# Performance work log

Measured on AMD Instinct MI355X. Metric: run time of the kernel, lower is better.

Reference implementation:

```python
import jax, jax.numpy as jnp
import numpy as np

B, S, E = 2, 2048, 2048
H, KV, D = 16, 4, 128


def setup_inputs() -> dict:
    key = jax.random.key(0)
    k0, k1, k2, k3, k4 = jax.random.split(key, 5)
    s = 0.02  # init scale for weights
    return {
        "x": jax.random.normal(k0, (B, S, E), jnp.float32),
        "wq": jax.random.normal(k1, (E, H * D), jnp.float32) * s,
        "wk": jax.random.normal(k2, (E, KV * D), jnp.float32) * s,
        "wv": jax.random.normal(k3, (E, KV * D), jnp.float32) * s,
        "wo": jax.random.normal(k4, (H * D, E), jnp.float32) * s,
    }


def _rope_tables(seq_len, head_dim, dtype):
    inv_freq = 1.0 / (10000.0 ** (jnp.arange(0, head_dim, 2, dtype=jnp.float32) / head_dim))
    t = jnp.arange(seq_len, dtype=jnp.float32)
    freqs = jnp.outer(t, inv_freq)  # [S, D/2]
    emb = jnp.concatenate([freqs, freqs], axis=-1)  # [S, D]
    cos = jnp.cos(emb).astype(dtype)[None, None]  # [1,1,S,D]
    sin = jnp.sin(emb).astype(dtype)[None, None]
    return cos, sin


def _rotate_half(x):
    x1, x2 = jnp.split(x, 2, axis=-1)
    return jnp.concatenate([-x2, x1], axis=-1)


def reference(x, wq, wk, wv, wo):
    b, s, _ = x.shape
    # projections -> [B, heads, S, D]
    q = (x @ wq).reshape(b, s, H, D).transpose(0, 2, 1, 3)
    k = (x @ wk).reshape(b, s, KV, D).transpose(0, 2, 1, 3)
    v = (x @ wv).reshape(b, s, KV, D).transpose(0, 2, 1, 3)
    # inline RoPE (rotate-half convention), applied to q and k
    cos, sin = _rope_tables(s, D, q.dtype)
    q = q * cos + _rotate_half(q) * sin
    k = k * cos + _rotate_half(k) * sin
    # GQA: duplicate K/V heads (repeat_interleave along head dim)
    rep = H // KV
    k = jnp.repeat(k, rep, axis=1)
    v = jnp.repeat(v, rep, axis=1)
    scale = 1.0 / np.sqrt(D)
    scores = jnp.einsum('bhqd,bhkd->bhqk', q, k) * scale  # [B,H,S,S]
    attn = jax.nn.softmax(scores.astype(jnp.float32), axis=-1).astype(q.dtype)
    out = jnp.einsum('bhqk,bhkd->bhqd', attn, v)  # [B,H,S,D]
    out = out.transpose(0, 2, 1, 3).reshape(b, s, H * D)
    return out @ wo
```

## Files before the change

kernel.cpp:

```cpp
#include <hip/hip_runtime.h>
#include <hip/hip_bf16.h>

typedef __attribute__((ext_vector_type(8))) short s16x8;
typedef __attribute__((ext_vector_type(4))) float f32x4;

__device__ inline float bf2f(unsigned short u) {
  union { unsigned int i; float f; } v; v.i = ((unsigned int)u) << 16; return v.f;
}
__device__ inline unsigned short f2bf(float f) {
  union { float f; unsigned int i; } v; v.f = f;
  unsigned int r = (v.i + 0x7FFFu + ((v.i >> 16) & 1u)) >> 16;
  return (unsigned short)r;
}
__device__ inline void gl_lds16(const void* g, void* l) {
  __builtin_amdgcn_global_load_lds(
      (const __attribute__((address_space(1))) unsigned int*)g,
      (__attribute__((address_space(3))) unsigned int*)l, 16, 0, 0);
}

__global__ __launch_bounds__(256) void cast_to_bf16(const float* __restrict__ s,
                                                    unsigned short* __restrict__ d, int n4) {
  int i = blockIdx.x * 256 + threadIdx.x;
  if (i >= n4) return;
  float4 v = ((const float4*)s)[i];
  ushort4 o;
  o.x = f2bf(v.x); o.y = f2bf(v.y); o.z = f2bf(v.z); o.w = f2bf(v.w);
  ((ushort4*)d)[i] = o;
}

__global__ __launch_bounds__(256) void transpose_cast(const float* __restrict__ src,
                                                      unsigned short* __restrict__ dst,
                                                      int K, int N) {
  __shared__ float tile[32][33];
  int n0 = blockIdx.x * 32, k0 = blockIdx.y * 32;
  int tx = threadIdx.x & 31, ty = threadIdx.x >> 5;
#pragma unroll
  for (int i = 0; i < 4; ++i) {
    int k = ty + i * 8;
    tile[k][tx] = src[(size_t)(k0 + k) * N + n0 + tx];
  }
  __syncthreads();
#pragma unroll
  for (int i = 0; i < 4; ++i) {
    int n = ty + i * 8;
    dst[(size_t)(n0 + n) * K + k0 + tx] = f2bf(tile[tx][n]);
  }
}

__global__ __launch_bounds__(256) void rope_tables(float* __restrict__ ct, float* __restrict__ st) {
  int idx = blockIdx.x * 256 + threadIdx.x;
  int s = idx >> 6, i = idx & 63;
  float inv = powf(10000.0f, -(float)(2 * i) * (1.0f / 128.0f));
  float ang = (float)s * inv;
  ct[idx] = cosf(ang);
  st[idx] = sinf(ang);
}

__global__ __launch_bounds__(256) void rope_apply(unsigned short* __restrict__ qkv,
                                                  const float* __restrict__ ct,
                                                  const float* __restrict__ st) {
  int row = blockIdx.x;
  int pos = row & 2047;
  unsigned short* base = qkv + (size_t)row * 3072;
  for (int it = threadIdx.x; it < 1280; it += 256) {
    int head = it >> 6, dh = it & 63;
    int col = head < 16 ? head * 128 : 2048 + (head - 16) * 128;
    float a = bf2f(base[col + dh]);
    float b = bf2f(base[col + dh + 64]);
    float c = ct[pos * 64 + dh], sn = st[pos * 64 + dh];
    base[col + dh] = f2bf(a * c - b * sn);
    base[col + dh + 64] = f2bf(b * c + a * sn);
  }
}

__global__ __launch_bounds__(256) void vtrans(const unsigned short* __restrict__ qkv,
                                              unsigned short* __restrict__ vt) {
  __shared__ unsigned short tile[32][33];
  int tx = threadIdx.x & 31, ty = threadIdx.x >> 5;
  int s0 = blockIdx.x * 32;
  int d0 = blockIdx.y * 32;
  int bz = blockIdx.z;
  const unsigned short* src = qkv + (size_t)((bz >> 2) * 2048) * 3072 + 2560 + (bz & 3) * 128;
#pragma unroll
  for (int i = 0; i < 4; ++i)
    tile[ty + i * 8][tx] = src[(size_t)(s0 + ty + i * 8) * 3072 + d0 + tx];
  __syncthreads();
  unsigned short* dst = vt + (size_t)bz * 128 * 2048;
#pragma unroll
  for (int i = 0; i < 4; ++i)
    dst[(size_t)(d0 + ty + i * 8) * 2048 + s0 + tx] = tile[tx][ty + i * 8];
}

template <int BF16OUT>
__global__ __launch_bounds__(512, 2) void gemm256(const unsigned short* __restrict__ A,
                                                  const unsigned short* __restrict__ BT,
                                                  void* __restrict__ Cv,
                                                  int M, int N, int K) {
  __shared__ __align__(16) unsigned short Lds[2][4][256 * 32];
  const int t = threadIdx.x, lane = t & 63;
  const int wid = t >> 6, m16 = lane & 15, l4 = lane >> 4;
  const int wm = wid >> 2, wn = wid & 3;
  const int swA = (l4 ^ ((m16 >> 1) & 3)) * 16;

  int gx = gridDim.x, nwg = gx * gridDim.y;
  int wg = blockIdx.y * gx + blockIdx.x;
  if ((nwg & 7) == 0) { int q = nwg >> 3; wg = (wg & 7) * q + (wg >> 3); }
  const int rowBase = (wg / gx) * 256, colBase = (wg % gx) * 256;

  const int r0 = t >> 2, c80 = (t & 3) ^ ((r0 >> 1) & 3);
  const int g1 = 512 + t, r1 = g1 >> 2, c81 = (g1 & 3) ^ ((r1 >> 1) & 3);
  const char* pA0 = (const char*)(A + (size_t)(rowBase + r0) * K + c80 * 8);
  const char* pA1 = (const char*)(A + (size_t)(rowBase + r1) * K + c81 * 8);
  const char* pB0 = (const char*)(BT + (size_t)(colBase + r0) * K + c80 * 8);
  const char* pB1 = (const char*)(BT + (size_t)(colBase + r1) * K + c81 * 8);

  f32x4 acc[8][4];
#pragma unroll
  for (int fr = 0; fr < 8; ++fr)
#pragma unroll
    for (int fn = 0; fn < 4; ++fn) {
      f32x4 z = {0.f, 0.f, 0.f, 0.f};
      acc[fr][fn] = z;
    }
  s16x8 bf[4];

#define STG(mat, kc, kt, buf)                                             \
  {                                                                       \
    size_t ko = (size_t)((kt) * 64 + (kc) * 32) * 2;                      \
    char* pl = (char*)&Lds[buf][(mat) * 2 + (kc)][0];                     \
    gl_lds16(((mat) ? pB0 : pA0) + ko, pl + t * 16);                      \
    gl_lds16(((mat) ? pB1 : pA1) + ko, pl + 8192 + t * 16);               \
  }

#define GATE()                                         \
  asm volatile("s_waitcnt vmcnt(8)" ::: "memory");     \
  __builtin_amdgcn_s_barrier();                        \
  __builtin_amdgcn_sched_barrier(0);

#define CMP(cur, kc, frh)                                                          \
  {                                                                                \
    const char* Ap = (const char*)&Lds[cur][kc][0];                                \
    s16x8 af[4];                                                                   \
    _Pragma("unroll") for (int i = 0; i < 4; ++i)                                  \
        af[i] = *(const s16x8*)(Ap + (wm * 128 + ((frh) * 4 + i) * 16 + m16) * 64 + swA); \
    if ((frh) == 0) {                                                              \
      const char* Bp = (const char*)&Lds[cur][2 + (kc)][0];                        \
      _Pragma("unroll") for (int n = 0; n < 4; ++n)                                \
          bf[n] = *(const s16x8*)(Bp + (wn * 64 + n * 16 + m16) * 64 + swA);       \
    }                                                                              \
    __builtin_amdgcn_s_setprio(1);                                                 \
    _Pragma("unroll") for (int i = 0; i < 4; ++i)                                  \
        _Pragma("unroll") for (int n = 0; n < 4; ++n)                              \
            acc[(frh) * 4 + i][n] = __builtin_amdgcn_mfma_f32_16x16x32_bf16(       \
                af[i], bf[n], acc[(frh) * 4 + i][n], 0, 0, 0);                     \
    __builtin_amdgcn_s_setprio(0);                                                 \
  }

  const int NT = K >> 6;
  STG(0, 0, 0, 0); STG(1, 0, 0, 0);
  STG(0, 1, 0, 0); STG(1, 1, 0, 0);
  STG(0, 0, 1, 1); STG(1, 0, 1, 1);

  for (int kt = 0; kt < NT; ++kt) {
    const int cur = kt & 1;
    GATE();
    if (kt + 1 < NT) STG(0, 1, kt + 1, cur ^ 1);
    CMP(cur, 0, 0);
    __builtin_amdgcn_s_barrier();
    if (kt + 1 < NT) STG(1, 1, kt + 1, cur ^ 1);
    CMP(cur, 0, 1);
    GATE();
    if (kt + 2 < NT) STG(0, 0, kt + 2, cur);
    CMP(cur, 1, 0);
    __builtin_amdgcn_s_barrier();
    if (kt + 2 < NT) STG(1, 0, kt + 2, cur);
    CMP(cur, 1, 1);
  }
#undef STG
#undef GATE
#undef CMP

#pragma unroll
  for (int fr = 0; fr < 8; ++fr)
#pragma unroll
    for (int fn = 0; fn < 4; ++fn) {
      int rr = rowBase + wm * 128 + fr * 16 + l4 * 4;
      int cc = colBase + wn * 64 + fn * 16 + m16;
#pragma unroll
      for (int jr = 0; jr < 4; ++jr) {
        if (BF16OUT)
          ((unsigned short*)Cv)[(size_t)(rr + jr) * N + cc] = f2bf(acc[fr][fn][jr]);
        else
          ((float*)Cv)[(size_t)(rr + jr) * N + cc] = acc[fr][fn][jr];
      }
    }
}

__global__ __launch_bounds__(512, 2) void gemm256_n128(const unsigned short* __restrict__ A,
                                                       const unsigned short* __restrict__ BT,
                                                       float* __restrict__ Cv,
                                                       int M, int N, int K) {
  __shared__ __align__(16) char Lds[98304];
  const int t = threadIdx.x, lane = t & 63;
  const int wid = t >> 6, m16 = lane & 15, l4 = lane >> 4;
  const int wm = wid >> 2, wn = wid & 3;
  const int swA = (l4 ^ ((m16 >> 1) & 3)) * 16;

  int gx = gridDim.x, nwg = gx * gridDim.y;
  int wg = blockIdx.y * gx + blockIdx.x;
  if ((nwg & 7) == 0) { int q = nwg >> 3; wg = (wg & 7) * q + (wg >> 3); }
  const int rowBase = (wg / gx) * 256, colBase = (wg % gx) * 128;

  const int r0 = t >> 2, c80 = (t & 3) ^ ((r0 >> 1) & 3);
  const int g1 = 512 + t, r1 = g1 >> 2, c81 = (g1 & 3) ^ ((r1 >> 1) & 3);
  const char* pA0 = (const char*)(A + (size_t)(rowBase + r0) * K + c80 * 8);
  const char* pA1 = (const char*)(A + (size_t)(rowBase + r1) * K + c81 * 8);
  const char* pB0 = (const char*)(BT + (size_t)(colBase + r0) * K + c80 * 8);

  f32x4 acc[8][2];
#pragma unroll
  for (int fr = 0; fr < 8; ++fr)
#pragma unroll
    for (int fn = 0; fn < 2; ++fn) {
      f32x4 z = {0.f, 0.f, 0.f, 0.f};
      acc[fr][fn] = z;
    }
  s16x8 bf[2];

#define ABASE(buf, kc) (Lds + (buf) * 49152 + (kc) * 16384)
#define BBASE(buf, kc) (Lds + (buf) * 49152 + 32768 + (kc) * 8192)

#define STGA(kc, kt, buf)                                                 \
  {                                                                       \
    size_t ko = (size_t)((kt) * 64 + (kc) * 32) * 2;                      \
    gl_lds16(pA0 + ko, ABASE(buf, kc) + t * 16);                          \
    gl_lds16(pA1 + ko, ABASE(buf, kc) + 8192 + t * 16);                   \
  }
#define STGB(kc, kt, buf)                                                 \
  {                                                                       \
    size_t ko = (size_t)((kt) * 64 + (kc) * 32) * 2;                      \
    gl_lds16(pB0 + ko, BBASE(buf, kc) + t * 16);                          \
  }

#define GATE()                                         \
  asm volatile("s_waitcnt vmcnt(6)" ::: "memory");     \
  __builtin_amdgcn_s_barrier();                        \
  __builtin_amdgcn_sched_barrier(0);

#define CMP(cur, kc, frh)                                                          \
  {                                                                                \
    const char* Ap = ABASE(cur, kc);                                               \
    s16x8 af[4];                                                                   \
    _Pragma("unroll") for (int i = 0; i < 4; ++i)                                  \
        af[i] = *(const s16x8*)(Ap + (wm * 128 + ((frh) * 4 + i) * 16 + m16) * 64 + swA); \
    if ((frh) == 0) {                                                              \
      const char* Bp = BBASE(cur, kc);                                             \
      _Pragma("unroll") for (int n = 0; n < 2; ++n)                                \
          bf[n] = *(const s16x8*)(Bp + (wn * 32 + n * 16 + m16) * 64 + swA);       \
    }                                                                              \
    __builtin_amdgcn_s_setprio(1);                                                 \
    _Pragma("unroll") for (int i = 0; i < 4; ++i)                                  \
        _Pragma("unroll") for (int n = 0; n < 2; ++n)                              \
            acc[(frh) * 4 + i][n] = __builtin_amdgcn_mfma_f32_16x16x32_bf16(       \
                af[i], bf[n], acc[(frh) * 4 + i][n], 0, 0, 0);                     \
    __builtin_amdgcn_s_setprio(0);                                                 \
  }

  const int NT = K >> 6;
  STGA(0, 0, 0); STGB(0, 0, 0);
  STGA(1, 0, 0); STGB(1, 0, 0);
  STGA(0, 1, 1); STGB(0, 1, 1);

  for (int kt = 0; kt < NT; ++kt) {
    const int cur = kt & 1;
    GATE();
    if (kt + 1 < NT) STGA(1, kt + 1, cur ^ 1);
    CMP(cur, 0, 0);
    __builtin_amdgcn_s_barrier();
    if (kt + 1 < NT) STGB(1, kt + 1, cur ^ 1);
    CMP(cur, 0, 1);
    GATE();
    if (kt + 2 < NT) STGA(0, kt + 2, cur);
    CMP(cur, 1, 0);
    __builtin_amdgcn_s_barrier();
    if (kt + 2 < NT) STGB(0, kt + 2, cur);
    CMP(cur, 1, 1);
  }
#undef STGA
#undef STGB
#undef GATE
#undef CMP
#undef ABASE
#undef BBASE

#pragma unroll
  for (int fr = 0; fr < 8; ++fr)
#pragma unroll
    for (int fn = 0; fn < 2; ++fn) {
      int rr = rowBase + wm * 128 + fr * 16 + l4 * 4;
      int cc = colBase + wn * 32 + fn * 16 + m16;
#pragma unroll
      for (int jr = 0; jr < 4; ++jr)
        Cv[(size_t)(rr + jr) * N + cc] = acc[fr][fn][jr];
    }
}

__global__ __launch_bounds__(256, 2) void attn_kernel(const unsigned short* __restrict__ qkv,
                                                      const unsigned short* __restrict__ vt,
                                                      unsigned short* __restrict__ obuf) {
  __shared__ __align__(16) unsigned short Kl[2][64 * 128];
  __shared__ __align__(16) unsigned short Vl[2][128 * 64];
  __shared__ __align__(16) unsigned short Pl[4][16 * 64];
  const int t = threadIdx.x, lane = t & 63, w = t >> 6;
  const int m16 = lane & 15, l4 = lane >> 4;
  const int b = blockIdx.z, h = blockIdx.y, qb = blockIdx.x;
  const int kvh = h >> 2;
  const float SCL = 0.12751744616570824f;

  s16x8 qf[2][4];
  {
    const unsigned short* qp =
        qkv + (size_t)(b * 2048 + qb * 128 + w * 32 + m16) * 3072 + h * 128 + l4 * 8;
#pragma unroll
    for (int qt = 0; qt < 2; ++qt)
#pragma unroll
      for (int dc = 0; dc < 4; ++dc)
        qf[qt][dc] = *(const s16x8*)(qp + qt * 16 * 3072 + dc * 32);
  }

  float lsum[2];
  f32x4 acco[2][8];
#pragma unroll
  for (int qt = 0; qt < 2; ++qt) lsum[qt] = 0.f;
#pragma unroll
  for (int qt = 0; qt < 2; ++qt)
#pragma unroll
    for (int df = 0; df < 8; ++df) {
      f32x4 z = {0.f, 0.f, 0.f, 0.f};
      acco[qt][df] = z;
    }

  const char* pK[4];
  const char* pV[4];
#pragma unroll
  for (int i = 0; i < 4; ++i) {
    int c = i * 256 + t;
    {
      int row = c >> 4, ch = c & 15;
      pK[i] = (const char*)(qkv + (size_t)(b * 2048 + row) * 3072 + 2048 + kvh * 128) +
              ((ch * 16) ^ ((row & 7) << 4));
    }
    {
      int d = c >> 3, ch = c & 7;
      pV[i] = (const char*)(vt + (size_t)((b * 4 + kvh) * 128 + d) * 2048) +
              ((ch * 16) ^ ((d & 7) << 4));
    }
  }
  const size_t KADV = (size_t)64 * 3072 * 2;
  const size_t VADV = 128;

#define STAGE_T(buf)                                                         \
  {                                                                          \
    _Pragma("unroll") for (int i = 0; i < 4; ++i)                            \
        gl_lds16(pK[i], (char*)Kl[buf] + (i * 256 + t) * 16);                \
    _Pragma("unroll") for (int i = 0; i < 4; ++i)                            \
        gl_lds16(pV[i], (char*)Vl[buf] + (i * 256 + t) * 16);                \
    _Pragma("unroll") for (int i = 0; i < 4; ++i) pK[i] += KADV;             \
    _Pragma("unroll") for (int i = 0; i < 4; ++i) pV[i] += VADV;             \
  }

  int cur = 0;
  STAGE_T(0);

  for (int kt = 0; kt < 32; ++kt) {
    if (kt < 31) {
      STAGE_T(cur ^ 1);
      asm volatile("s_waitcnt vmcnt(8)" ::: "memory");
    } else {
      asm volatile("s_waitcnt vmcnt(0)" ::: "memory");
    }
    __builtin_amdgcn_s_barrier();
    __builtin_amdgcn_sched_barrier(0);

    f32x4 sc[2][4];
#pragma unroll
    for (int qt = 0; qt < 2; ++qt)
#pragma unroll
      for (int kkt = 0; kkt < 4; ++kkt) {
        f32x4 z = {0.f, 0.f, 0.f, 0.f};
        sc[qt][kkt] = z;
      }
    __builtin_amdgcn_s_setprio(1);
#pragma unroll
    for (int kkt = 0; kkt < 4; ++kkt) {
      int row = kkt * 16 + m16;
      const char* kr = (const char*)Kl[cur] + row * 256;
      int sw = (row & 7) << 4;
#pragma unroll
      for (int dc = 0; dc < 4; ++dc) {
        s16x8 kf = *(const s16x8*)(kr + ((dc * 64 + l4 * 16) ^ sw));
        sc[0][kkt] = __builtin_amdgcn_mfma_f32_16x16x32_bf16(kf, qf[0][dc], sc[0][kkt], 0, 0, 0);
        sc[1][kkt] = __builtin_amdgcn_mfma_f32_16x16x32_bf16(kf, qf[1][dc], sc[1][kkt], 0, 0, 0);
      }
    }
    __builtin_amdgcn_s_setprio(0);

    s16x8 ap[2][2];
#pragma unroll
    for (int qt = 0; qt < 2; ++qt) {
      char* pr = (char*)Pl[w] + m16 * 128;
      int swp = (m16 & 7) << 4;
      float part = 0.f;
#pragma unroll
      for (int kkt = 0; kkt < 4; ++kkt) {
        float x0 = sc[qt][kkt][0] * SCL;
        float x1 = sc[qt][kkt][1] * SCL;
        float x2 = sc[qt][kkt][2] * SCL;
        float x3 = sc[qt][kkt][3] * SCL;
        float e0, e1, e2, e3;
        asm("v_exp_f32 %0, %1" : "=v"(e0) : "v"(x0));
        asm("v_exp_f32 %0, %1" : "=v"(e1) : "v"(x1));
        asm("v_exp_f32 %0, %1" : "=v"(e2) : "v"(x2));
        asm("v_exp_f32 %0, %1" : "=v"(e3) : "v"(x3));
        part += (e0 + e1) + (e2 + e3);
        unsigned int r01, r23;
        asm("v_cvt_pk_bf16_f32 %0, %1, %2" : "=v"(r01) : "v"(e0), "v"(e1));
        asm("v_cvt_pk_bf16_f32 %0, %1, %2" : "=v"(r23) : "v"(e2), "v"(e3));
        uint2 pw;
        pw.x = r01; pw.y = r23;
        *(uint2*)(pr + ((kkt * 32 + l4 * 8) ^ swp)) = pw;
      }
      lsum[qt] += part;
#pragma unroll
      for (int kc = 0; kc < 2; ++kc)
        ap[qt][kc] = *(const s16x8*)((const char*)Pl[w] + m16 * 128 +
                                     ((kc * 64 + l4 * 16) ^ ((m16 & 7) << 4)));
    }

    __builtin_amdgcn_s_setprio(1);
#pragma unroll
    for (int df = 0; df < 8; ++df) {
      int d = df * 16 + m16;
      const char* vr = (const char*)Vl[cur] + d * 128;
      int swv = (d & 7) << 4;
      s16x8 vf0 = *(const s16x8*)(vr + ((l4 * 16) ^ swv));
      s16x8 vf1 = *(const s16x8*)(vr + ((64 + l4 * 16) ^ swv));
      acco[0][df] = __builtin_amdgcn_mfma_f32_16x16x32_bf16(ap[0][0], vf0, acco[0][df], 0, 0, 0);
      acco[0][df] = __builtin_amdgcn_mfma_f32_16x16x32_bf16(ap[0][1], vf1, acco[0][df], 0, 0, 0);
      acco[1][df] = __builtin_amdgcn_mfma_f32_16x16x32_bf16(ap[1][0], vf0, acco[1][df], 0, 0, 0);
      acco[1][df] = __builtin_amdgcn_mfma_f32_16x16x32_bf16(ap[1][1], vf1, acco[1][df], 0, 0, 0);
    }
    __builtin_amdgcn_s_setprio(0);
    __builtin_amdgcn_s_barrier();
    cur ^= 1;
  }
#undef STAGE_T

#pragma unroll
  for (int qt = 0; qt < 2; ++qt) {
    float s = lsum[qt];
    s += __shfl_xor(s, 16);
    s += __shfl_xor(s, 32);
    float iv = 1.0f / s;
    unsigned short* op = obuf +
        (size_t)(b * 2048 + qb * 128 + w * 32 + qt * 16 + l4 * 4) * 2048 + h * 128 + m16;
#pragma unroll
    for (int jr = 0; jr < 4; ++jr) {
      float ivj = __shfl(iv, l4 * 4 + jr);
#pragma unroll
      for (int df = 0; df < 8; ++df)
        op[(size_t)jr * 2048 + df * 16] = f2bf(acco[qt][df][jr] * ivj);
    }
  }
}

extern "C" void kernel_launch(void* const* d_in, const int* in_sizes, int n_in,
                              void* d_out, int out_size, void* d_ws, size_t ws_size,
                              hipStream_t stream) {
  (void)in_sizes; (void)n_in; (void)out_size; (void)ws_size;
  const float* x  = (const float*)d_in[0];
  const float* wq = (const float*)d_in[1];
  const float* wk = (const float*)d_in[2];
  const float* wv = (const float*)d_in[3];
  const float* wo = (const float*)d_in[4];

  char* ws = (char*)d_ws;
  unsigned short* xb    = (unsigned short*)(ws);
  unsigned short* wqkvT = (unsigned short*)(ws + 16777216);
  unsigned short* woT   = (unsigned short*)(ws + 29360128);
  unsigned short* qkv   = (unsigned short*)(ws + 37748736);
  unsigned short* obuf  = (unsigned short*)(ws + 62914560);
  float* ct             = (float*)(ws + 79691776);
  float* st             = (float*)(ws + 80216064);
  unsigned short* vt    = xb;

  cast_to_bf16<<<8192, 256, 0, stream>>>(x, xb, 2097152);
  transpose_cast<<<dim3(64, 64), 256, 0, stream>>>(wq, wqkvT, 2048, 2048);
  transpose_cast<<<dim3(16, 64), 256, 0, stream>>>(wk, wqkvT + 2048 * 2048, 2048, 512);
  transpose_cast<<<dim3(16, 64), 256, 0, stream>>>(wv, wqkvT + 2560 * 2048, 2048, 512);
  transpose_cast<<<dim3(64, 64), 256, 0, stream>>>(wo, woT, 2048, 2048);
  rope_tables<<<512, 256, 0, stream>>>(ct, st);
  gemm256<1><<<dim3(12, 16), 512, 0, stream>>>(xb, wqkvT, qkv, 4096, 3072, 2048);
  rope_apply<<<4096, 256, 0, stream>>>(qkv, ct, st);
  vtrans<<<dim3(64, 4, 8), 256, 0, stream>>>(qkv, vt);
  attn_kernel<<<dim3(16, 16, 2), 256, 0, stream>>>(qkv, vt, obuf);
  gemm256_n128<<<dim3(16, 16), 512, 0, stream>>>(obuf, woT, (float*)d_out, 4096, 2048, 2048);
}
```

Measured before the change: 209.8 us.

## Switch attention MFMAs to 32x32x16 and keep P in registers via permlane swap

Rewrites the attention inner loop to use 32x32x16 bf16 MFMAs, computing S^T so each lane holds one query's scores. The exp'd probabilities are repacked into B-operand fragments with v_permlane32_swap instead of a round trip through per-wave shared memory. This removes the P LDS store/load and halves the K/V fragment reads per MFMA work, at the cost of larger accumulators (more VGPRs) and a different output write pattern.

```diff
diff --git a/kernel.cpp b/kernel.cpp
--- a/kernel.cpp
+++ b/kernel.cpp
@@ -3,6 +3,7 @@
 
 typedef __attribute__((ext_vector_type(8))) short s16x8;
 typedef __attribute__((ext_vector_type(4))) float f32x4;
+typedef __attribute__((ext_vector_type(16))) float f32x16;
 
 __device__ inline float bf2f(unsigned short u) {
   union { unsigned int i; float f; } v; v.i = ((unsigned int)u) << 16; return v.f;
@@ -310,35 +311,24 @@
                                                       unsigned short* __restrict__ obuf) {
   __shared__ __align__(16) unsigned short Kl[2][64 * 128];
   __shared__ __align__(16) unsigned short Vl[2][128 * 64];
-  __shared__ __align__(16) unsigned short Pl[4][16 * 64];
   const int t = threadIdx.x, lane = t & 63, w = t >> 6;
-  const int m16 = lane & 15, l4 = lane >> 4;
+  const int q32 = lane & 31, l32 = lane >> 5;
   const int b = blockIdx.z, h = blockIdx.y, qb = blockIdx.x;
   const int kvh = h >> 2;
   const float SCL = 0.12751744616570824f;
 
-  s16x8 qf[2][4];
+  s16x8 qf[8];
   {
     const unsigned short* qp =
-        qkv + (size_t)(b * 2048 + qb * 128 + w * 32 + m16) * 3072 + h * 128 + l4 * 8;
-#pragma unroll
-    for (int qt = 0; qt < 2; ++qt)
-#pragma unroll
-      for (int dc = 0; dc < 4; ++dc)
-        qf[qt][dc] = *(const s16x8*)(qp + qt * 16 * 3072 + dc * 32);
-  }
-
-  float lsum[2];
-  f32x4 acco[2][8];
-#pragma unroll
-  for (int qt = 0; qt < 2; ++qt) lsum[qt] = 0.f;
-#pragma unroll
-  for (int qt = 0; qt < 2; ++qt)
-#pragma unroll
-    for (int df = 0; df < 8; ++df) {
-      f32x4 z = {0.f, 0.f, 0.f, 0.f};
-      acco[qt][df] = z;
-    }
+        qkv + (size_t)(b * 2048 + qb * 128 + w * 32 + q32) * 3072 + h * 128 + l32 * 8;
+#pragma unroll
+    for (int ds = 0; ds < 8; ++ds) qf[ds] = *(const s16x8*)(qp + ds * 16);
+  }
+
+  float lsum = 0.f;
+  f32x16 acco[4];
+#pragma unroll
+  for (int dt = 0; dt < 4; ++dt) acco[dt] = (f32x16){};
 
   const char* pK[4];
   const char* pV[4];
@@ -382,73 +372,67 @@
     __builtin_amdgcn_s_barrier();
     __builtin_amdgcn_sched_barrier(0);
 
-    f32x4 sc[2][4];
-#pragma unroll
-    for (int qt = 0; qt < 2; ++qt)
-#pragma unroll
-      for (int kkt = 0; kkt < 4; ++kkt) {
-        f32x4 z = {0.f, 0.f, 0.f, 0.f};
-        sc[qt][kkt] = z;
-      }
+    f32x16 sc32[2];
     __builtin_amdgcn_s_setprio(1);
 #pragma unroll
-    for (int kkt = 0; kkt < 4; ++kkt) {
-      int row = kkt * 16 + m16;
-      const char* kr = (const char*)Kl[cur] + row * 256;
-      int sw = (row & 7) << 4;
-#pragma unroll
-      for (int dc = 0; dc < 4; ++dc) {
-        s16x8 kf = *(const s16x8*)(kr + ((dc * 64 + l4 * 16) ^ sw));
-        sc[0][kkt] = __builtin_amdgcn_mfma_f32_16x16x32_bf16(kf, qf[0][dc], sc[0][kkt], 0, 0, 0);
-        sc[1][kkt] = __builtin_amdgcn_mfma_f32_16x16x32_bf16(kf, qf[1][dc], sc[1][kkt], 0, 0, 0);
-      }
+    for (int kt32 = 0; kt32 < 2; ++kt32) {
+      f32x16 a = (f32x16){};
+      int r = kt32 * 32 + q32;
+      const char* kr = (const char*)Kl[cur] + r * 256;
+      int sw = (r & 7) << 4;
+#pragma unroll
+      for (int ds = 0; ds < 8; ++ds) {
+        s16x8 kf = *(const s16x8*)(kr + ((ds * 32 + l32 * 16) ^ sw));
+        a = __builtin_amdgcn_mfma_f32_32x32x16_bf16(kf, qf[ds], a, 0, 0, 0);
+      }
+      sc32[kt32] = a;
     }
     __builtin_amdgcn_s_setprio(0);
 
-    s16x8 ap[2][2];
-#pragma unroll
-    for (int qt = 0; qt < 2; ++qt) {
-      char* pr = (char*)Pl[w] + m16 * 128;
-      int swp = (m16 & 7) << 4;
-      float part = 0.f;
-#pragma unroll
-      for (int kkt = 0; kkt < 4; ++kkt) {
-        float x0 = sc[qt][kkt][0] * SCL;
-        float x1 = sc[qt][kkt][1] * SCL;
-        float x2 = sc[qt][kkt][2] * SCL;
-        float x3 = sc[qt][kkt][3] * SCL;
-        float e0, e1, e2, e3;
-        asm("v_exp_f32 %0, %1" : "=v"(e0) : "v"(x0));
-        asm("v_exp_f32 %0, %1" : "=v"(e1) : "v"(x1));
-        asm("v_exp_f32 %0, %1" : "=v"(e2) : "v"(x2));
-        asm("v_exp_f32 %0, %1" : "=v"(e3) : "v"(x3));
-        part += (e0 + e1) + (e2 + e3);
-        unsigned int r01, r23;
-        asm("v_cvt_pk_bf16_f32 %0, %1, %2" : "=v"(r01) : "v"(e0), "v"(e1));
-        asm("v_cvt_pk_bf16_f32 %0, %1, %2" : "=v"(r23) : "v"(e2), "v"(e3));
-        uint2 pw;
-        pw.x = r01; pw.y = r23;
-        *(uint2*)(pr + ((kkt * 32 + l4 * 8) ^ swp)) = pw;
-      }
-      lsum[qt] += part;
-#pragma unroll
-      for (int kc = 0; kc < 2; ++kc)
-        ap[qt][kc] = *(const s16x8*)((const char*)Pl[w] + m16 * 128 +
-                                     ((kc * 64 + l4 * 16) ^ ((m16 & 7) << 4)));
-    }
+    s16x8 bfrag[4];
+    float part = 0.f;
+#pragma unroll
+    for (int kt32 = 0; kt32 < 2; ++kt32) {
+      float e[16];
+#pragma unroll
+      for (int rg = 0; rg < 16; ++rg) {
+        float x = sc32[kt32][rg] * SCL;
+        asm("v_exp_f32 %0, %1" : "=v"(e[rg]) : "v"(x));
+      }
+#pragma unroll
+      for (int rg = 0; rg < 16; ++rg) part += e[rg];
+      unsigned int pr[4][2];
+#pragma unroll
+      for (int a2 = 0; a2 < 4; ++a2) {
+        asm("v_cvt_pk_bf16_f32 %0, %1, %2"
+            : "=v"(pr[a2][0]) : "v"(e[a2 * 4 + 0]), "v"(e[a2 * 4 + 1]));
+        asm("v_cvt_pk_bf16_f32 %0, %1, %2"
+            : "=v"(pr[a2][1]) : "v"(e[a2 * 4 + 2]), "v"(e[a2 * 4 + 3]));
+      }
+#pragma unroll
+      for (int hf = 0; hf < 2; ++hf) {
+        unsigned int x0 = pr[2 * hf][0], y0 = pr[2 * hf + 1][0];
+        unsigned int x1 = pr[2 * hf][1], y1 = pr[2 * hf + 1][1];
+        asm("v_permlane32_swap_b32 %0, %1" : "+v"(x0), "+v"(y0));
+        asm("v_permlane32_swap_b32 %0, %1" : "+v"(x1), "+v"(y1));
+        union { unsigned int u[4]; s16x8 v; } bb;
+        bb.u[0] = x0; bb.u[1] = x1; bb.u[2] = y0; bb.u[3] = y1;
+        bfrag[kt32 * 2 + hf] = bb.v;
+      }
+    }
+    lsum += part;
 
     __builtin_amdgcn_s_setprio(1);
 #pragma unroll
-    for (int df = 0; df < 8; ++df) {
-      int d = df * 16 + m16;
+    for (int dt = 0; dt < 4; ++dt) {
+      int d = dt * 32 + q32;
       const char* vr = (const char*)Vl[cur] + d * 128;
       int swv = (d & 7) << 4;
-      s16x8 vf0 = *(const s16x8*)(vr + ((l4 * 16) ^ swv));
-      s16x8 vf1 = *(const s16x8*)(vr + ((64 + l4 * 16) ^ swv));
-      acco[0][df] = __builtin_amdgcn_mfma_f32_16x16x32_bf16(ap[0][0], vf0, acco[0][df], 0, 0, 0);
-      acco[0][df] = __builtin_amdgcn_mfma_f32_16x16x32_bf16(ap[0][1], vf1, acco[0][df], 0, 0, 0);
-      acco[1][df] = __builtin_amdgcn_mfma_f32_16x16x32_bf16(ap[1][0], vf0, acco[1][df], 0, 0, 0);
-      acco[1][df] = __builtin_amdgcn_mfma_f32_16x16x32_bf16(ap[1][1], vf1, acco[1][df], 0, 0, 0);
+#pragma unroll
+      for (int ts = 0; ts < 4; ++ts) {
+        s16x8 vf = *(const s16x8*)(vr + ((ts * 32 + l32 * 16) ^ swv));
+        acco[dt] = __builtin_amdgcn_mfma_f32_32x32x16_bf16(vf, bfrag[ts], acco[dt], 0, 0, 0);
+      }
     }
     __builtin_amdgcn_s_setprio(0);
     __builtin_amdgcn_s_barrier();
@@ -456,21 +440,19 @@
   }
 #undef STAGE_T
 
-#pragma unroll
-  for (int qt = 0; qt < 2; ++qt) {
-    float s = lsum[qt];
-    s += __shfl_xor(s, 16);
+  {
+    float s = lsum;
     s += __shfl_xor(s, 32);
     float iv = 1.0f / s;
-    unsigned short* op = obuf +
-        (size_t)(b * 2048 + qb * 128 + w * 32 + qt * 16 + l4 * 4) * 2048 + h * 128 + m16;
-#pragma unroll
-    for (int jr = 0; jr < 4; ++jr) {
-      float ivj = __shfl(iv, l4 * 4 + jr);
-#pragma unroll
-      for (int df = 0; df < 8; ++df)
-        op[(size_t)jr * 2048 + df * 16] = f2bf(acco[qt][df][jr] * ivj);
-    }
+    unsigned short* op =
+        obuf + (size_t)(b * 2048 + qb * 128 + w * 32 + q32) * 2048 + h * 128;
+#pragma unroll
+    for (int dt = 0; dt < 4; ++dt)
+#pragma unroll
+      for (int rg = 0; rg < 16; ++rg) {
+        int d = dt * 32 + (rg & 3) + 8 * (rg >> 2) + 4 * l32;
+        op[d] = f2bf(acco[dt][rg] * iv);
+      }
   }
 }
 
```

Result: slower. 214.0 us (+2.0%).
